# Kernel optimization log

Hardware: AMD Instinct MI355X
Metric: run time of the kernel (lower is better)

## Reference

```python
import jax, jax.numpy as jnp
import numpy as np

B, N, S, F = 16384, 1152, 576, 8  # batch, n_sites, n_symm, features
LOG2 = float(np.log(2.0))


def log_cosh(x):
    # numerically stable log(cosh(x)) = |x| + log1p(exp(-2|x|)) - log(2)
    a = jnp.abs(x)
    return a + jnp.log1p(jnp.exp(-2.0 * a)) - LOG2


def setup_inputs() -> dict:
    key = jax.random.key(0)
    ks = iter(jax.random.split(key, 32))
    f32 = jnp.float32
    d = {}
    d['x'] = jax.random.normal(next(ks), (B, N), dtype=f32)
    d['symmetries'] = jax.random.randint(next(ks), (S, N), 0, N, dtype=jnp.int32)
    d['corr0'] = jax.random.randint(next(ks), (576, 4), 0, N, dtype=jnp.int32)
    d['corr1'] = jax.random.randint(next(ks), (576, 4), 0, N, dtype=jnp.int32)
    d['corr2'] = jax.random.randint(next(ks), (24, 24), 0, N, dtype=jnp.int32)
    d['corr3'] = jax.random.randint(next(ks), (24, 24), 0, N, dtype=jnp.int32)
    d['corr0_symm'] = jax.random.randint(next(ks), (S, 576), 0, 576, dtype=jnp.int32)
    d['corr1_symm'] = jax.random.randint(next(ks), (S, 576), 0, 576, dtype=jnp.int32)
    d['corr2_symm'] = jax.random.randint(next(ks), (S, 24), 0, 24, dtype=jnp.int32)
    d['corr3_symm'] = jax.random.randint(next(ks), (S, 24), 0, 24, dtype=jnp.int32)
    std = 0.01
    d['hidden_bias'] = std * jax.random.normal(next(ks), (F,), dtype=f32)
    d['symm_kernel'] = std * jax.random.normal(next(ks), (F, N), dtype=f32)
    d['visible_bias'] = std * jax.random.normal(next(ks), (2,), dtype=f32)
    d['corr0_bias'] = std * jax.random.normal(next(ks), (1,), dtype=f32)
    d['corr0_kernel'] = std * jax.random.normal(next(ks), (F, 576), dtype=f32)
    d['corr1_bias'] = std * jax.random.normal(next(ks), (1,), dtype=f32)
    d['corr1_kernel'] = std * jax.random.normal(next(ks), (F, 576), dtype=f32)
    d['corr2_bias'] = std * jax.random.normal(next(ks), (1,), dtype=f32)
    d['corr2_kernel'] = std * jax.random.normal(next(ks), (F, 24), dtype=f32)
    d['corr3_bias'] = std * jax.random.normal(next(ks), (1,), dtype=f32)
    d['corr3_kernel'] = std * jax.random.normal(next(ks), (F, 24), dtype=f32)
    d['loop0_hidden_bias'] = std * jax.random.normal(next(ks), (F,), dtype=f32)
    d['loop0_kernel'] = std * jax.random.normal(next(ks), (F, 24), dtype=f32)
    d['loop1_hidden_bias'] = std * jax.random.normal(next(ks), (F,), dtype=f32)
    d['loop1_kernel'] = std * jax.random.normal(next(ks), (F, 24), dtype=f32)
    return d


def reference(x, symmetries, corr0, corr1, corr2, corr3,
              corr0_symm, corr1_symm, corr2_symm, corr3_symm,
              hidden_bias, symm_kernel, visible_bias,
              corr0_bias, corr0_kernel, corr1_bias, corr1_kernel,
              corr2_bias, corr2_kernel, corr3_bias, corr3_kernel,
              loop0_hidden_bias, loop0_kernel, loop1_hidden_bias, loop1_kernel):
    n_batch = x.shape[0]
    # symmetrized kernel: (F, S, N)
    K = jnp.take(symm_kernel, symmetries, axis=1)
    theta = jnp.einsum('bn,fsn->bfs', x, K)  # (B, F, S)
    theta = theta + hidden_bias[:, None]
    bias = jnp.sum(x.reshape(n_batch, -1, 2), axis=1) @ visible_bias  # (B,)

    correlators = [corr0, corr1, corr2, corr3]
    corr_symms = [corr0_symm, corr1_symm, corr2_symm, corr3_symm]
    corr_biases = [corr0_bias, corr1_bias, corr2_bias, corr3_bias]
    corr_kernels = [corr0_kernel, corr1_kernel, corr2_kernel, corr3_kernel]

    corr_values = []
    for corr, csym, cb, ck in zip(correlators, corr_symms, corr_biases, corr_kernels):
        ckk = jnp.take(ck, csym, axis=1)               # (F, S, C)
        cv = jnp.take(x, corr, axis=1).prod(axis=2)    # (B, C)
        corr_values.append(cv)
        theta = theta + jnp.einsum('bc,fsc->bfs', cv, ckk)
        bias = bias + cb * jnp.sum(cv, axis=1)

    out = jnp.sum(log_cosh(theta), axis=(1, 2))  # (B,)

    # last two correlators are loop correlators with dedicated hidden units
    loop_params = [(loop0_hidden_bias, loop0_kernel, corr2_symm, corr_values[2]),
                   (loop1_hidden_bias, loop1_kernel, corr3_symm, corr_values[3])]
    for lhb, lk, lsym, lv in loop_params:
        lkk = jnp.take(lk, lsym, axis=1)                      # (F, S, C)
        lt = jnp.einsum('bc,fsc->bfs', lv, lkk) + lhb[:, None]
        out = out + jnp.sum(log_cosh(lt), axis=(1, 2))

    return out + bias
```

## Files before the change

kernel.cpp:

```cpp
#include <hip/hip_runtime.h>
#include <math.h>

#define B_    16384
#define N_    1152
#define KPAD  2496
#define KLOOP 256
#define NOUT  4608
#define NT    36
#define LOG2F_ 0.69314718055994530942f

typedef unsigned short ushort_t;
typedef __attribute__((ext_vector_type(8))) short short8;
typedef __attribute__((ext_vector_type(4))) float floatx4;

__device__ __forceinline__ float log_cosh_f(float t) {
    float a = fabsf(t);
    return a + __logf(1.0f + __expf(-2.0f * a)) - LOG2F_;
}
__device__ __forceinline__ ushort_t bf16_rne(float f) {
    unsigned int u = __float_as_uint(f);
    return (ushort_t)((u + 0x7fffu + ((u >> 16) & 1u)) >> 16);
}
__device__ __forceinline__ float bf16_to_f(ushort_t h) {
    return __uint_as_float(((unsigned int)h) << 16);
}

typedef __attribute__((address_space(1))) const unsigned int guint;
typedef __attribute__((address_space(3))) unsigned int luint;
__device__ __forceinline__ void gload16(const ushort_t* src, ushort_t* dst) {
    __builtin_amdgcn_global_load_lds((guint*)src, (luint*)dst, 16, 0, 0);
}

__global__ __launch_bounds__(256) void build_w(
    const int* __restrict__ symm,
    const int* __restrict__ c0s, const int* __restrict__ c1s,
    const int* __restrict__ c2s, const int* __restrict__ c3s,
    const float* __restrict__ sk,
    const float* __restrict__ ck0, const float* __restrict__ ck1,
    const float* __restrict__ ck2, const float* __restrict__ ck3,
    const float* __restrict__ l0k, const float* __restrict__ l1k,
    ushort_t* __restrict__ Wb, ushort_t* __restrict__ LWb)
{
    __shared__ int idx[2352];
    const int s = blockIdx.x;
    const int tid = threadIdx.x;
    for (int i = tid; i < 1152; i += 256) idx[i] = symm[s * N_ + i];
    for (int i = tid; i < 576; i += 256) idx[1152 + i] = c0s[s * 576 + i];
    for (int i = tid; i < 576; i += 256) idx[1728 + i] = c1s[s * 576 + i];
    if (tid < 24) idx[2304 + tid] = c2s[s * 24 + tid];
    else if (tid < 48) idx[2328 + (tid - 24)] = c3s[s * 24 + (tid - 24)];
    __syncthreads();
    for (int f = 0; f < 8; ++f) {
        ushort_t* wr = Wb + (size_t)(s * 8 + f) * KPAD;
        for (int k = tid; k < KPAD; k += 256) {
            ushort_t o;
            if (k < 1152)      o = bf16_rne(sk[f * N_ + idx[k]]);
            else if (k < 1728) o = bf16_rne(ck0[f * 576 + idx[k]]);
            else if (k < 2304) o = bf16_rne(ck1[f * 576 + idx[k]]);
            else if (k < 2448) {
                int q = k - 2304, g = q / 48, c = q - g * 48;
                float w = (c < 24) ? ck2[f * 24 + idx[2304 + c]]
                                   : ck3[f * 24 + idx[2328 + (c - 24)]];
                ushort_t hi = bf16_rne(w);
                o = (g < 2) ? hi : bf16_rne(w - bf16_to_f(hi));
            } else o = 0;
            wr[k] = o;
        }
        ushort_t* lr = LWb + (size_t)(s * 8 + f) * KLOOP;
        for (int k2 = tid; k2 < KLOOP; k2 += 256) {
            int j2 = k2 >> 7, q = k2 & 127;
            ushort_t o = 0;
            if (q < 72) {
                int g = q / 24, c = q - g * 24;
                float w = j2 ? l1k[f * 24 + idx[2328 + c]]
                             : l0k[f * 24 + idx[2304 + c]];
                ushort_t hi = bf16_rne(w);
                o = (g < 2) ? hi : bf16_rne(w - bf16_to_f(hi));
            }
            lr[k2] = o;
        }
    }
}

__global__ __launch_bounds__(256) void build_cv(
    const float* __restrict__ x,
    const int* __restrict__ corr0, const int* __restrict__ corr1,
    const int* __restrict__ corr2, const int* __restrict__ corr3,
    const float* __restrict__ vb,
    const float* __restrict__ cb0, const float* __restrict__ cb1,
    const float* __restrict__ cb2, const float* __restrict__ cb3,
    ushort_t* __restrict__ XA, ushort_t* __restrict__ CVL,
    float* __restrict__ initb)
{
    __shared__ float xs[N_];
    __shared__ float red[256];
    __shared__ float cvhi[48], cvlo[48];
    const int tid = threadIdx.x;
    const int b = blockIdx.x;
    ushort_t* xr = XA + (size_t)b * KPAD;

    float bias = 0.f;
    const float vb0 = vb[0], vb1 = vb[1];
    for (int i = tid; i < N_; i += 256) {
        float v = x[(size_t)b * N_ + i];
        xs[i] = v;
        bias += v * ((i & 1) ? vb1 : vb0);
        xr[i] = bf16_rne(v);
    }
    __syncthreads();
    float s0 = 0.f, s1 = 0.f, s2 = 0.f, s3 = 0.f;
    for (int c = tid; c < 576; c += 256) {
        const int* i0 = corr0 + c * 4;
        float p = xs[i0[0]] * xs[i0[1]] * xs[i0[2]] * xs[i0[3]];
        xr[1152 + c] = bf16_rne(p); s0 += p;
        const int* i1 = corr1 + c * 4;
        float q = xs[i1[0]] * xs[i1[1]] * xs[i1[2]] * xs[i1[3]];
        xr[1728 + c] = bf16_rne(q); s1 += q;
    }
    if (tid < 48) {
        int j2 = tid / 24, c = tid - j2 * 24;
        const int* ii = (j2 ? corr3 : corr2) + c * 24;
        float p = 1.f;
        for (int j = 0; j < 24; ++j) p *= xs[ii[j]];
        float hv = bf16_to_f(bf16_rne(p));
        cvhi[tid] = hv;
        cvlo[tid] = p - hv;
        if (j2) s3 = p; else s2 = p;
    }
    __syncthreads();
    for (int i = tid; i < KPAD - 2304; i += 256) {
        ushort_t o = 0;
        if (i < 144) {
            int g = i / 48, c = i - g * 48;
            o = bf16_rne(g == 1 ? cvlo[c] : cvhi[c]);
        }
        xr[2304 + i] = o;
    }
    ushort_t* cr = CVL + (size_t)b * KLOOP;
    for (int k2 = tid; k2 < KLOOP; k2 += 256) {
        int j2 = k2 >> 7, q = k2 & 127;
        ushort_t o = 0;
        if (q < 72) {
            int g = q / 24, c = q - g * 24;
            o = bf16_rne(g == 1 ? cvlo[j2 * 24 + c] : cvhi[j2 * 24 + c]);
        }
        cr[k2] = o;
    }
    bias += cb0[0] * s0 + cb1[0] * s1 + cb2[0] * s2 + cb3[0] * s3;
    red[tid] = bias;
    __syncthreads();
    for (int off = 128; off; off >>= 1) {
        if (tid < off) red[tid] += red[tid + off];
        __syncthreads();
    }
    if (tid == 0) initb[b] = red[0];
}

__global__ __launch_bounds__(256, 2) void mfma_gemm(
    const ushort_t* __restrict__ XA, const ushort_t* __restrict__ Wb,
    const ushort_t* __restrict__ CVL, const ushort_t* __restrict__ LWb,
    const float* __restrict__ hidden_bias,
    const float* __restrict__ l0hb, const float* __restrict__ l1hb,
    float* __restrict__ partials)
{
    __shared__ __align__(16) ushort_t sh[32768];
    __shared__ float redsh[384];

    const int tid = threadIdx.x;
    const int l = tid & 63, w = tid >> 6;
    const int wm = w >> 1, wn = w & 1;
    const int lrow = l & 15, lg = l >> 4;
    const int sgr = ((tid & 3) ^ ((tid >> 3) & 3)) * 8;
    const int srow = tid >> 2;
    const int wb512 = w * 512;

    const int bid = blockIdx.x;
    const int swz = (bid & 7) * 576 + (bid >> 3);
    const int nt = swz >> 7, bt = swz & 127;
    const int n0 = nt * 128, b0 = bt * 128;

    const ushort_t* pA0 = XA + (size_t)(b0 + srow) * KPAD + sgr;
    const ushort_t* pA1 = pA0 + (size_t)64 * KPAD;
    const ushort_t* pB0 = Wb + (size_t)(n0 + srow) * KPAD + sgr;
    const ushort_t* pB1 = pB0 + (size_t)64 * KPAD;

    const int oct = (lg ^ ((lrow >> 1) & 3)) * 8;
    const int aoff = (wm * 64 + lrow) * 32 + oct;
    const int boff = 4096 + (wn * 64 + lrow) * 32 + oct;

    floatx4 acc[4][4];
    short8 RA[8], RB[8];

    auto STG = [&](int bufUS, int offUS) {
        gload16(pA0 + offUS, &sh[bufUS + 0    + wb512]);
        gload16(pA1 + offUS, &sh[bufUS + 2048 + wb512]);
        gload16(pB0 + offUS, &sh[bufUS + 4096 + wb512]);
        gload16(pB1 + offUS, &sh[bufUS + 6144 + wb512]);
    };
    auto RD = [&](int bufUS, short8* R) {
#pragma unroll
        for (int mi = 0; mi < 4; ++mi)
            R[mi] = *(const short8*)&sh[bufUS + aoff + mi * 512];
#pragma unroll
        for (int ni = 0; ni < 4; ++ni)
            R[4 + ni] = *(const short8*)&sh[bufUS + boff + ni * 512];
    };
    auto MM = [&](short8* R) {
        __builtin_amdgcn_s_setprio(1);
#pragma unroll
        for (int mi = 0; mi < 4; ++mi)
#pragma unroll
            for (int ni = 0; ni < 4; ++ni)
                acc[mi][ni] = __builtin_amdgcn_mfma_f32_16x16x32_bf16(
                    R[mi], R[4 + ni], acc[mi][ni], 0, 0, 0);
        __builtin_amdgcn_s_setprio(0);
    };
#define PIPE_BAR() do { asm volatile("s_waitcnt vmcnt(4)" ::: "memory"); \
    __builtin_amdgcn_s_barrier(); } while (0)

#pragma unroll
    for (int mi = 0; mi < 4; ++mi)
#pragma unroll
        for (int ni = 0; ni < 4; ++ni) acc[mi][ni] = (floatx4){0.f, 0.f, 0.f, 0.f};

    STG(0, 0); STG(8192, 32); STG(16384, 64);
    asm volatile("s_waitcnt vmcnt(8)" ::: "memory");
    __builtin_amdgcn_s_barrier();
    RD(0, RA);

#pragma unroll 1
    for (int m = 0; m < 19; ++m) {
        RD(8192, RB);  STG(24576, 96);
        __builtin_amdgcn_sched_barrier(0);
        MM(RA); PIPE_BAR();
        RD(16384, RA); STG(0, 128);
        __builtin_amdgcn_sched_barrier(0);
        MM(RB); PIPE_BAR();
        RD(24576, RB); STG(8192, 160);
        __builtin_amdgcn_sched_barrier(0);
        MM(RA); PIPE_BAR();
        RD(0, RA);     STG(16384, 192);
        __builtin_amdgcn_sched_barrier(0);
        MM(RB); PIPE_BAR();
        pA0 += 128; pA1 += 128; pB0 += 128; pB1 += 128;
    }
    RD(8192, RB);
    __builtin_amdgcn_sched_barrier(0);
    MM(RA);
    MM(RB);

    {
        const float hbv = hidden_bias[l & 7];
#pragma unroll
        for (int mi = 0; mi < 4; ++mi)
#pragma unroll
            for (int reg = 0; reg < 4; ++reg) {
                float v = 0.f;
#pragma unroll
                for (int ni = 0; ni < 4; ++ni)
                    v += log_cosh_f(acc[mi][ni][reg] + hbv);
                v += __shfl_xor(v, 1); v += __shfl_xor(v, 2);
                v += __shfl_xor(v, 4); v += __shfl_xor(v, 8);
                if (lrow == 0)
                    redsh[(wm * 64 + mi * 16 + lg * 4 + reg) * 3 + wn] = v;
            }
    }

    const ushort_t* pC0 = CVL + (size_t)(b0 + srow) * KLOOP + sgr;
    const ushort_t* pC1 = pC0 + (size_t)64 * KLOOP;
    const ushort_t* pL0 = LWb + (size_t)(n0 + srow) * KLOOP + sgr;
    const ushort_t* pL1 = pL0 + (size_t)64 * KLOOP;
    auto STGm = [&](int bufUS, int offUS) {
        gload16(pC0 + offUS, &sh[bufUS + 0    + wb512]);
        gload16(pC1 + offUS, &sh[bufUS + 2048 + wb512]);
        gload16(pL0 + offUS, &sh[bufUS + 4096 + wb512]);
        gload16(pL1 + offUS, &sh[bufUS + 6144 + wb512]);
    };
#pragma unroll
    for (int j2 = 0; j2 < 2; ++j2) {
#pragma unroll
        for (int mi = 0; mi < 4; ++mi)
#pragma unroll
            for (int ni = 0; ni < 4; ++ni) acc[mi][ni] = (floatx4){0.f, 0.f, 0.f, 0.f};
        __syncthreads();
        const int kb = j2 * 128;
        STGm(0, kb); STGm(8192, kb + 32); STGm(16384, kb + 64); STGm(24576, kb + 96);
        __syncthreads();
        RD(0, RA);     MM(RA);
        RD(8192, RB);  MM(RB);
        RD(16384, RA); MM(RA);
        RD(24576, RB); MM(RB);
        const float lbv = (j2 ? l1hb : l0hb)[l & 7];
#pragma unroll
        for (int mi = 0; mi < 4; ++mi)
#pragma unroll
            for (int reg = 0; reg < 4; ++reg) {
                float v = 0.f;
#pragma unroll
                for (int ni = 0; ni < 4; ++ni)
                    v += log_cosh_f(acc[mi][ni][reg] + lbv);
                v += __shfl_xor(v, 1); v += __shfl_xor(v, 2);
                v += __shfl_xor(v, 4); v += __shfl_xor(v, 8);
                if (lrow == 0)
                    redsh[(wm * 64 + mi * 16 + lg * 4 + reg) * 3 + wn] += v;
            }
    }

    __syncthreads();
    if (tid < 128) {
        float t = redsh[tid * 3 + 0] + redsh[tid * 3 + 1];
        partials[(size_t)nt * B_ + b0 + tid] = t;
    }
#undef PIPE_BAR
}

__global__ __launch_bounds__(256) void finalize_out(
    const float* __restrict__ initb, const float* __restrict__ partials,
    float* __restrict__ out)
{
    int b = blockIdx.x * 256 + threadIdx.x;
    float s = initb[b];
#pragma unroll
    for (int t = 0; t < NT; ++t) s += partials[(size_t)t * B_ + b];
    out[b] = s;
}

extern "C" void kernel_launch(void* const* d_in, const int* in_sizes, int n_in,
                              void* d_out, int out_size, void* d_ws, size_t ws_size,
                              hipStream_t stream) {
    const float* x    = (const float*)d_in[0];
    const int* symm   = (const int*)d_in[1];
    const int* corr0  = (const int*)d_in[2];
    const int* corr1  = (const int*)d_in[3];
    const int* corr2  = (const int*)d_in[4];
    const int* corr3  = (const int*)d_in[5];
    const int* c0s    = (const int*)d_in[6];
    const int* c1s    = (const int*)d_in[7];
    const int* c2s    = (const int*)d_in[8];
    const int* c3s    = (const int*)d_in[9];
    const float* hb   = (const float*)d_in[10];
    const float* sk   = (const float*)d_in[11];
    const float* vb   = (const float*)d_in[12];
    const float* cb0  = (const float*)d_in[13];
    const float* ck0  = (const float*)d_in[14];
    const float* cb1  = (const float*)d_in[15];
    const float* ck1  = (const float*)d_in[16];
    const float* cb2  = (const float*)d_in[17];
    const float* ck2  = (const float*)d_in[18];
    const float* cb3  = (const float*)d_in[19];
    const float* ck3  = (const float*)d_in[20];
    const float* l0hb = (const float*)d_in[21];
    const float* l0k  = (const float*)d_in[22];
    const float* l1hb = (const float*)d_in[23];
    const float* l1k  = (const float*)d_in[24];

    ushort_t* wsu = (ushort_t*)d_ws;
    ushort_t* Wb  = wsu;
    ushort_t* XA  = Wb + (size_t)NOUT * KPAD;
    ushort_t* LWb = XA + (size_t)B_ * KPAD;
    ushort_t* CVL = LWb + (size_t)NOUT * KLOOP;
    float* initb    = (float*)(CVL + (size_t)B_ * KLOOP);
    float* partials = initb + B_;

    build_w<<<576, 256, 0, stream>>>(
        symm, c0s, c1s, c2s, c3s, sk, ck0, ck1, ck2, ck3, l0k, l1k, Wb, LWb);
    build_cv<<<B_, 256, 0, stream>>>(
        x, corr0, corr1, corr2, corr3, vb, cb0, cb1, cb2, cb3, XA, CVL, initb);
    mfma_gemm<<<4608, 256, 0, stream>>>(
        XA, Wb, CVL, LWb, hb, l0hb, l1hb, partials);
    finalize_out<<<B_ / 256, 256, 0, stream>>>(initb, partials, (float*)d_out);
}
```

Baseline: 670.2 us.

## Enlarge GEMM block tile to 256x128 with triple-buffered LDS pipeline

The MFMA GEMM block tile grows from 128x128 to 256x128 (batch x outputs). Each wave now holds 8x4 accumulators and the grid halves to 2304 blocks. The prefetch pipeline changes from four to three LDS buffers with one barrier per k-step, and the LDS swizzle for staging is adjusted. The goal is more arithmetic per byte loaded and fewer barriers. In exchange it doubles accumulator registers and may lower occupancy under the launch bound of 2.

```diff
diff --git a/kernel.cpp b/kernel.cpp
--- a/kernel.cpp
+++ b/kernel.cpp
@@ -163,96 +163,86 @@
     const float* __restrict__ l0hb, const float* __restrict__ l1hb,
     float* __restrict__ partials)
 {
-    __shared__ __align__(16) ushort_t sh[32768];
-    __shared__ float redsh[384];
+    __shared__ __align__(16) ushort_t sh[36864];
+    __shared__ float redsh[768];
 
     const int tid = threadIdx.x;
     const int l = tid & 63, w = tid >> 6;
     const int wm = w >> 1, wn = w & 1;
     const int lrow = l & 15, lg = l >> 4;
-    const int sgr = ((tid & 3) ^ ((tid >> 3) & 3)) * 8;
     const int srow = tid >> 2;
+    const int sgr = ((tid & 3) ^ ((srow >> 1) & 3)) * 8;
     const int wb512 = w * 512;
 
     const int bid = blockIdx.x;
-    const int swz = (bid & 7) * 576 + (bid >> 3);
-    const int nt = swz >> 7, bt = swz & 127;
-    const int n0 = nt * 128, b0 = bt * 128;
-
-    const ushort_t* pA0 = XA + (size_t)(b0 + srow) * KPAD + sgr;
-    const ushort_t* pA1 = pA0 + (size_t)64 * KPAD;
-    const ushort_t* pB0 = Wb + (size_t)(n0 + srow) * KPAD + sgr;
-    const ushort_t* pB1 = pB0 + (size_t)64 * KPAD;
+    const int swz = (bid & 7) * 288 + (bid >> 3);
+    const int nt = swz >> 6, bt = swz & 63;
+    const int n0 = nt * 128, b0 = bt * 256;
+
+    const ushort_t* pa0 = XA + (size_t)(b0 + srow) * KPAD + sgr;
+    const ushort_t* pa1 = pa0 + (size_t)64 * KPAD;
+    const ushort_t* pa2 = pa0 + (size_t)128 * KPAD;
+    const ushort_t* pa3 = pa0 + (size_t)192 * KPAD;
+    const ushort_t* pb0 = Wb + (size_t)(n0 + srow) * KPAD + sgr;
+    const ushort_t* pb1 = pb0 + (size_t)64 * KPAD;
 
     const int oct = (lg ^ ((lrow >> 1) & 3)) * 8;
-    const int aoff = (wm * 64 + lrow) * 32 + oct;
-    const int boff = 4096 + (wn * 64 + lrow) * 32 + oct;
-
-    floatx4 acc[4][4];
-    short8 RA[8], RB[8];
-
-    auto STG = [&](int bufUS, int offUS) {
-        gload16(pA0 + offUS, &sh[bufUS + 0    + wb512]);
-        gload16(pA1 + offUS, &sh[bufUS + 2048 + wb512]);
-        gload16(pB0 + offUS, &sh[bufUS + 4096 + wb512]);
-        gload16(pB1 + offUS, &sh[bufUS + 6144 + wb512]);
+    const int aoff = (wm * 128 + lrow) * 32 + oct;
+    const int boff = 8192 + (wn * 64 + lrow) * 32 + oct;
+
+    floatx4 acc[8][4];
+
+    auto STAGE = [&](int buf, int off) {
+        gload16(pa0 + off, &sh[buf + 0    + wb512]);
+        gload16(pa1 + off, &sh[buf + 2048 + wb512]);
+        gload16(pa2 + off, &sh[buf + 4096 + wb512]);
+        gload16(pa3 + off, &sh[buf + 6144 + wb512]);
+        gload16(pb0 + off, &sh[buf + 8192 + wb512]);
+        gload16(pb1 + off, &sh[buf + 10240 + wb512]);
     };
-    auto RD = [&](int bufUS, short8* R) {
-#pragma unroll
-        for (int mi = 0; mi < 4; ++mi)
-            R[mi] = *(const short8*)&sh[bufUS + aoff + mi * 512];
+    auto TILE = [&](int buf) {
+        short8 af[8], bf[4];
+#pragma unroll
+        for (int mi = 0; mi < 8; ++mi)
+            af[mi] = *(const short8*)&sh[buf + aoff + mi * 512];
 #pragma unroll
         for (int ni = 0; ni < 4; ++ni)
-            R[4 + ni] = *(const short8*)&sh[bufUS + boff + ni * 512];
-    };
-    auto MM = [&](short8* R) {
+            bf[ni] = *(const short8*)&sh[buf + boff + ni * 512];
         __builtin_amdgcn_s_setprio(1);
 #pragma unroll
-        for (int mi = 0; mi < 4; ++mi)
+        for (int mi = 0; mi < 8; ++mi)
 #pragma unroll
             for (int ni = 0; ni < 4; ++ni)
                 acc[mi][ni] = __builtin_amdgcn_mfma_f32_16x16x32_bf16(
-                    R[mi], R[4 + ni], acc[mi][ni], 0, 0, 0);
+                    af[mi], bf[ni], acc[mi][ni], 0, 0, 0);
         __builtin_amdgcn_s_setprio(0);
     };
-#define PIPE_BAR() do { asm volatile("s_waitcnt vmcnt(4)" ::: "memory"); \
+#define VMB(N) do { asm volatile("s_waitcnt vmcnt(" #N ")" ::: "memory"); \
     __builtin_amdgcn_s_barrier(); } while (0)
-
-#pragma unroll
-    for (int mi = 0; mi < 4; ++mi)
+#define SB0() __builtin_amdgcn_sched_barrier(0)
+
+#pragma unroll
+    for (int mi = 0; mi < 8; ++mi)
 #pragma unroll
         for (int ni = 0; ni < 4; ++ni) acc[mi][ni] = (floatx4){0.f, 0.f, 0.f, 0.f};
 
-    STG(0, 0); STG(8192, 32); STG(16384, 64);
-    asm volatile("s_waitcnt vmcnt(8)" ::: "memory");
-    __builtin_amdgcn_s_barrier();
-    RD(0, RA);
+    STAGE(0, 0); STAGE(12288, 32);
 
 #pragma unroll 1
-    for (int m = 0; m < 19; ++m) {
-        RD(8192, RB);  STG(24576, 96);
-        __builtin_amdgcn_sched_barrier(0);
-        MM(RA); PIPE_BAR();
-        RD(16384, RA); STG(0, 128);
-        __builtin_amdgcn_sched_barrier(0);
-        MM(RB); PIPE_BAR();
-        RD(24576, RB); STG(8192, 160);
-        __builtin_amdgcn_sched_barrier(0);
-        MM(RA); PIPE_BAR();
-        RD(0, RA);     STG(16384, 192);
-        __builtin_amdgcn_sched_barrier(0);
-        MM(RB); PIPE_BAR();
-        pA0 += 128; pA1 += 128; pB0 += 128; pB1 += 128;
-    }
-    RD(8192, RB);
-    __builtin_amdgcn_sched_barrier(0);
-    MM(RA);
-    MM(RB);
+    for (int m = 0; m < 25; ++m) {
+        VMB(6); STAGE(24576, 64);  SB0(); TILE(0);
+        VMB(6); STAGE(0, 96);      SB0(); TILE(12288);
+        VMB(6); STAGE(12288, 128); SB0(); TILE(24576);
+        pa0 += 96; pa1 += 96; pa2 += 96; pa3 += 96; pb0 += 96; pb1 += 96;
+    }
+    VMB(6); STAGE(24576, 64); SB0(); TILE(0);
+    VMB(6); TILE(12288);
+    VMB(0); TILE(24576);
 
     {
         const float hbv = hidden_bias[l & 7];
 #pragma unroll
-        for (int mi = 0; mi < 4; ++mi)
+        for (int mi = 0; mi < 8; ++mi)
 #pragma unroll
             for (int reg = 0; reg < 4; ++reg) {
                 float v = 0.f;
@@ -262,37 +252,42 @@
                 v += __shfl_xor(v, 1); v += __shfl_xor(v, 2);
                 v += __shfl_xor(v, 4); v += __shfl_xor(v, 8);
                 if (lrow == 0)
-                    redsh[(wm * 64 + mi * 16 + lg * 4 + reg) * 3 + wn] = v;
+                    redsh[(wm * 128 + mi * 16 + lg * 4 + reg) * 3 + wn] = v;
             }
     }
 
-    const ushort_t* pC0 = CVL + (size_t)(b0 + srow) * KLOOP + sgr;
-    const ushort_t* pC1 = pC0 + (size_t)64 * KLOOP;
-    const ushort_t* pL0 = LWb + (size_t)(n0 + srow) * KLOOP + sgr;
-    const ushort_t* pL1 = pL0 + (size_t)64 * KLOOP;
-    auto STGm = [&](int bufUS, int offUS) {
-        gload16(pC0 + offUS, &sh[bufUS + 0    + wb512]);
-        gload16(pC1 + offUS, &sh[bufUS + 2048 + wb512]);
-        gload16(pL0 + offUS, &sh[bufUS + 4096 + wb512]);
-        gload16(pL1 + offUS, &sh[bufUS + 6144 + wb512]);
+    const ushort_t* pc0 = CVL + (size_t)(b0 + srow) * KLOOP + sgr;
+    const ushort_t* pc1 = pc0 + (size_t)64 * KLOOP;
+    const ushort_t* pc2 = pc0 + (size_t)128 * KLOOP;
+    const ushort_t* pc3 = pc0 + (size_t)192 * KLOOP;
+    const ushort_t* pl0 = LWb + (size_t)(n0 + srow) * KLOOP + sgr;
+    const ushort_t* pl1 = pl0 + (size_t)64 * KLOOP;
+    auto STGm = [&](int buf, int off) {
+        gload16(pc0 + off, &sh[buf + 0    + wb512]);
+        gload16(pc1 + off, &sh[buf + 2048 + wb512]);
+        gload16(pc2 + off, &sh[buf + 4096 + wb512]);
+        gload16(pc3 + off, &sh[buf + 6144 + wb512]);
+        gload16(pl0 + off, &sh[buf + 8192 + wb512]);
+        gload16(pl1 + off, &sh[buf + 10240 + wb512]);
     };
 #pragma unroll
     for (int j2 = 0; j2 < 2; ++j2) {
 #pragma unroll
-        for (int mi = 0; mi < 4; ++mi)
+        for (int mi = 0; mi < 8; ++mi)
 #pragma unroll
             for (int ni = 0; ni < 4; ++ni) acc[mi][ni] = (floatx4){0.f, 0.f, 0.f, 0.f};
         __syncthreads();
         const int kb = j2 * 128;
-        STGm(0, kb); STGm(8192, kb + 32); STGm(16384, kb + 64); STGm(24576, kb + 96);
-        __syncthreads();
-        RD(0, RA);     MM(RA);
-        RD(8192, RB);  MM(RB);
-        RD(16384, RA); MM(RA);
-        RD(24576, RB); MM(RB);
+        STGm(0, kb); STGm(12288, kb + 32); STGm(24576, kb + 64);
+        __syncthreads();
+        TILE(0); TILE(12288);
+        __syncthreads();
+        STGm(0, kb + 96);
+        __syncthreads();
+        TILE(24576); TILE(0);
         const float lbv = (j2 ? l1hb : l0hb)[l & 7];
 #pragma unroll
-        for (int mi = 0; mi < 4; ++mi)
+        for (int mi = 0; mi < 8; ++mi)
 #pragma unroll
             for (int reg = 0; reg < 4; ++reg) {
                 float v = 0.f;
@@ -302,16 +297,17 @@
                 v += __shfl_xor(v, 1); v += __shfl_xor(v, 2);
                 v += __shfl_xor(v, 4); v += __shfl_xor(v, 8);
                 if (lrow == 0)
-                    redsh[(wm * 64 + mi * 16 + lg * 4 + reg) * 3 + wn] += v;
+                    redsh[(wm * 128 + mi * 16 + lg * 4 + reg) * 3 + wn] += v;
             }
     }
 
     __syncthreads();
-    if (tid < 128) {
+    {
         float t = redsh[tid * 3 + 0] + redsh[tid * 3 + 1];
         partials[(size_t)nt * B_ + b0 + tid] = t;
     }
-#undef PIPE_BAR
+#undef VMB
+#undef SB0
 }
 
 __global__ __launch_bounds__(256) void finalize_out(
@@ -366,7 +362,7 @@
         symm, c0s, c1s, c2s, c3s, sk, ck0, ck1, ck2, ck3, l0k, l1k, Wb, LWb);
     build_cv<<<B_, 256, 0, stream>>>(
         x, corr0, corr1, corr2, corr3, vb, cb0, cb1, cb2, cb3, XA, CVL, initb);
-    mfma_gemm<<<4608, 256, 0, stream>>>(
+    mfma_gemm<<<2304, 256, 0, stream>>>(
         XA, Wb, CVL, LWb, hb, l0hb, l1hb, partials);
     finalize_out<<<B_ / 256, 256, 0, stream>>>(initb, partials, (float*)d_out);
 }
```

Result: faster. 625.2 us (-6.7%).

## Restructure GEMM to 512 threads, 2x4 wave grid, double-buffered shallow pipeline

Applied to the files above, without the earlier changes.

The main MFMA GEMM moves from 256 threads with a 2x2 wave layout (64x64 per wave) and a 4-stage LDS ring to 512 threads with a 2x4 layout (64x32 per wave) and a 2-buffer pipeline. LDS per block drops to 32KB and launch bounds ask for 6 blocks per CU. The aim is fewer registers and less LDS per wave so more waves are resident to hide latency. In exchange, each loop step now waits with vmcnt(0) and a barrier, so there is less load/compute overlap inside a block, and the smaller per-wave tile lowers register-level data reuse.

```diff
diff --git a/kernel.cpp b/kernel.cpp
--- a/kernel.cpp
+++ b/kernel.cpp
@@ -156,22 +156,21 @@
     if (tid == 0) initb[b] = red[0];
 }
 
-__global__ __launch_bounds__(256, 2) void mfma_gemm(
+__global__ __launch_bounds__(512, 6) void mfma_gemm(
     const ushort_t* __restrict__ XA, const ushort_t* __restrict__ Wb,
     const ushort_t* __restrict__ CVL, const ushort_t* __restrict__ LWb,
     const float* __restrict__ hidden_bias,
     const float* __restrict__ l0hb, const float* __restrict__ l1hb,
     float* __restrict__ partials)
 {
-    __shared__ __align__(16) ushort_t sh[32768];
-    __shared__ float redsh[384];
+    __shared__ __align__(16) ushort_t sh[16384];
+    __shared__ float redsh[640];
 
     const int tid = threadIdx.x;
     const int l = tid & 63, w = tid >> 6;
-    const int wm = w >> 1, wn = w & 1;
+    const int wm = w >> 2, wn = w & 3;
     const int lrow = l & 15, lg = l >> 4;
     const int sgr = ((tid & 3) ^ ((tid >> 3) & 3)) * 8;
-    const int srow = tid >> 2;
     const int wb512 = w * 512;
 
     const int bid = blockIdx.x;
@@ -179,75 +178,53 @@
     const int nt = swz >> 7, bt = swz & 127;
     const int n0 = nt * 128, b0 = bt * 128;
 
-    const ushort_t* pA0 = XA + (size_t)(b0 + srow) * KPAD + sgr;
-    const ushort_t* pA1 = pA0 + (size_t)64 * KPAD;
-    const ushort_t* pB0 = Wb + (size_t)(n0 + srow) * KPAD + sgr;
-    const ushort_t* pB1 = pB0 + (size_t)64 * KPAD;
+    const ushort_t* pa = XA + (size_t)(b0 + (tid >> 2)) * KPAD + sgr;
+    const ushort_t* pb = Wb + (size_t)(n0 + (tid >> 2)) * KPAD + sgr;
 
     const int oct = (lg ^ ((lrow >> 1) & 3)) * 8;
     const int aoff = (wm * 64 + lrow) * 32 + oct;
-    const int boff = 4096 + (wn * 64 + lrow) * 32 + oct;
-
-    floatx4 acc[4][4];
-    short8 RA[8], RB[8];
-
-    auto STG = [&](int bufUS, int offUS) {
-        gload16(pA0 + offUS, &sh[bufUS + 0    + wb512]);
-        gload16(pA1 + offUS, &sh[bufUS + 2048 + wb512]);
-        gload16(pB0 + offUS, &sh[bufUS + 4096 + wb512]);
-        gload16(pB1 + offUS, &sh[bufUS + 6144 + wb512]);
+    const int boff = 4096 + (wn * 32 + lrow) * 32 + oct;
+
+    floatx4 acc[4][2];
+
+    auto STAGE = [&](int buf, int koff) {
+        gload16(pa + koff, &sh[buf + wb512]);
+        gload16(pb + koff, &sh[buf + 4096 + wb512]);
     };
-    auto RD = [&](int bufUS, short8* R) {
-#pragma unroll
-        for (int mi = 0; mi < 4; ++mi)
-            R[mi] = *(const short8*)&sh[bufUS + aoff + mi * 512];
-#pragma unroll
-        for (int ni = 0; ni < 4; ++ni)
-            R[4 + ni] = *(const short8*)&sh[bufUS + boff + ni * 512];
-    };
-    auto MM = [&](short8* R) {
+    auto TILE = [&](int buf) {
+        short8 af[4], bf[2];
+#pragma unroll
+        for (int mi = 0; mi < 4; ++mi)
+            af[mi] = *(const short8*)&sh[buf + aoff + mi * 512];
+#pragma unroll
+        for (int ni = 0; ni < 2; ++ni)
+            bf[ni] = *(const short8*)&sh[buf + boff + ni * 512];
         __builtin_amdgcn_s_setprio(1);
 #pragma unroll
         for (int mi = 0; mi < 4; ++mi)
 #pragma unroll
-            for (int ni = 0; ni < 4; ++ni)
+            for (int ni = 0; ni < 2; ++ni)
                 acc[mi][ni] = __builtin_amdgcn_mfma_f32_16x16x32_bf16(
-                    R[mi], R[4 + ni], acc[mi][ni], 0, 0, 0);
+                    af[mi], bf[ni], acc[mi][ni], 0, 0, 0);
         __builtin_amdgcn_s_setprio(0);
     };
-#define PIPE_BAR() do { asm volatile("s_waitcnt vmcnt(4)" ::: "memory"); \
+#define VM0B() do { asm volatile("s_waitcnt vmcnt(0)" ::: "memory"); \
     __builtin_amdgcn_s_barrier(); } while (0)
+#define SB0() __builtin_amdgcn_sched_barrier(0)
 
 #pragma unroll
     for (int mi = 0; mi < 4; ++mi)
 #pragma unroll
-        for (int ni = 0; ni < 4; ++ni) acc[mi][ni] = (floatx4){0.f, 0.f, 0.f, 0.f};
-
-    STG(0, 0); STG(8192, 32); STG(16384, 64);
-    asm volatile("s_waitcnt vmcnt(8)" ::: "memory");
-    __builtin_amdgcn_s_barrier();
-    RD(0, RA);
-
+        for (int ni = 0; ni < 2; ++ni) acc[mi][ni] = (floatx4){0.f, 0.f, 0.f, 0.f};
+
+    STAGE(0, 0);
 #pragma unroll 1
-    for (int m = 0; m < 19; ++m) {
-        RD(8192, RB);  STG(24576, 96);
-        __builtin_amdgcn_sched_barrier(0);
-        MM(RA); PIPE_BAR();
-        RD(16384, RA); STG(0, 128);
-        __builtin_amdgcn_sched_barrier(0);
-        MM(RB); PIPE_BAR();
-        RD(24576, RB); STG(8192, 160);
-        __builtin_amdgcn_sched_barrier(0);
-        MM(RA); PIPE_BAR();
-        RD(0, RA);     STG(16384, 192);
-        __builtin_amdgcn_sched_barrier(0);
-        MM(RB); PIPE_BAR();
-        pA0 += 128; pA1 += 128; pB0 += 128; pB1 += 128;
-    }
-    RD(8192, RB);
-    __builtin_amdgcn_sched_barrier(0);
-    MM(RA);
-    MM(RB);
+    for (int m = 0; m < 39; ++m) {
+        VM0B(); STAGE(8192, 32); SB0(); TILE(0);
+        VM0B(); if (m < 38) STAGE(0, 64);
+        SB0();  TILE(8192);
+        pa += 64; pb += 64;
+    }
 
     {
         const float hbv = hidden_bias[l & 7];
@@ -255,63 +232,58 @@
         for (int mi = 0; mi < 4; ++mi)
 #pragma unroll
             for (int reg = 0; reg < 4; ++reg) {
-                float v = 0.f;
-#pragma unroll
-                for (int ni = 0; ni < 4; ++ni)
-                    v += log_cosh_f(acc[mi][ni][reg] + hbv);
+                float v = log_cosh_f(acc[mi][0][reg] + hbv)
+                        + log_cosh_f(acc[mi][1][reg] + hbv);
                 v += __shfl_xor(v, 1); v += __shfl_xor(v, 2);
                 v += __shfl_xor(v, 4); v += __shfl_xor(v, 8);
                 if (lrow == 0)
-                    redsh[(wm * 64 + mi * 16 + lg * 4 + reg) * 3 + wn] = v;
+                    redsh[(wm * 64 + mi * 16 + lg * 4 + reg) * 5 + wn] = v;
             }
     }
 
-    const ushort_t* pC0 = CVL + (size_t)(b0 + srow) * KLOOP + sgr;
-    const ushort_t* pC1 = pC0 + (size_t)64 * KLOOP;
-    const ushort_t* pL0 = LWb + (size_t)(n0 + srow) * KLOOP + sgr;
-    const ushort_t* pL1 = pL0 + (size_t)64 * KLOOP;
-    auto STGm = [&](int bufUS, int offUS) {
-        gload16(pC0 + offUS, &sh[bufUS + 0    + wb512]);
-        gload16(pC1 + offUS, &sh[bufUS + 2048 + wb512]);
-        gload16(pL0 + offUS, &sh[bufUS + 4096 + wb512]);
-        gload16(pL1 + offUS, &sh[bufUS + 6144 + wb512]);
+    const ushort_t* pc = CVL + (size_t)(b0 + (tid >> 2)) * KLOOP + sgr;
+    const ushort_t* pl = LWb + (size_t)(n0 + (tid >> 2)) * KLOOP + sgr;
+    auto STGm = [&](int buf, int koff) {
+        gload16(pc + koff, &sh[buf + wb512]);
+        gload16(pl + koff, &sh[buf + 4096 + wb512]);
     };
 #pragma unroll
     for (int j2 = 0; j2 < 2; ++j2) {
 #pragma unroll
         for (int mi = 0; mi < 4; ++mi)
 #pragma unroll
-            for (int ni = 0; ni < 4; ++ni) acc[mi][ni] = (floatx4){0.f, 0.f, 0.f, 0.f};
+            for (int ni = 0; ni < 2; ++ni) acc[mi][ni] = (floatx4){0.f, 0.f, 0.f, 0.f};
         __syncthreads();
         const int kb = j2 * 128;
-        STGm(0, kb); STGm(8192, kb + 32); STGm(16384, kb + 64); STGm(24576, kb + 96);
-        __syncthreads();
-        RD(0, RA);     MM(RA);
-        RD(8192, RB);  MM(RB);
-        RD(16384, RA); MM(RA);
-        RD(24576, RB); MM(RB);
+        STGm(0, kb); STGm(8192, kb + 32);
+        __syncthreads();
+        TILE(0); TILE(8192);
+        __syncthreads();
+        STGm(0, kb + 64); STGm(8192, kb + 96);
+        __syncthreads();
+        TILE(0); TILE(8192);
         const float lbv = (j2 ? l1hb : l0hb)[l & 7];
 #pragma unroll
         for (int mi = 0; mi < 4; ++mi)
 #pragma unroll
             for (int reg = 0; reg < 4; ++reg) {
-                float v = 0.f;
-#pragma unroll
-                for (int ni = 0; ni < 4; ++ni)
-                    v += log_cosh_f(acc[mi][ni][reg] + lbv);
+                float v = log_cosh_f(acc[mi][0][reg] + lbv)
+                        + log_cosh_f(acc[mi][1][reg] + lbv);
                 v += __shfl_xor(v, 1); v += __shfl_xor(v, 2);
                 v += __shfl_xor(v, 4); v += __shfl_xor(v, 8);
                 if (lrow == 0)
-                    redsh[(wm * 64 + mi * 16 + lg * 4 + reg) * 3 + wn] += v;
+                    redsh[(wm * 64 + mi * 16 + lg * 4 + reg) * 5 + wn] += v;
             }
     }
 
     __syncthreads();
     if (tid < 128) {
-        float t = redsh[tid * 3 + 0] + redsh[tid * 3 + 1];
+        float t = redsh[tid * 5 + 0] + redsh[tid * 5 + 1] +
+                  redsh[tid * 5 + 2] + redsh[tid * 5 + 3];
         partials[(size_t)nt * B_ + b0 + tid] = t;
     }
-#undef PIPE_BAR
+#undef VM0B
+#undef SB0
 }
 
 __global__ __launch_bounds__(256) void finalize_out(
@@ -366,7 +338,7 @@
         symm, c0s, c1s, c2s, c3s, sk, ck0, ck1, ck2, ck3, l0k, l1k, Wb, LWb);
     build_cv<<<B_, 256, 0, stream>>>(
         x, corr0, corr1, corr2, corr3, vb, cb0, cb1, cb2, cb3, XA, CVL, initb);
-    mfma_gemm<<<4608, 256, 0, stream>>>(
+    mfma_gemm<<<4608, 512, 0, stream>>>(
         XA, Wb, CVL, LWb, hb, l0hb, l1hb, partials);
     finalize_out<<<B_ / 256, 256, 0, stream>>>(initb, partials, (float*)d_out);
 }
```

Result: faster. 646.3 us (-3.6%).
